# Kernel tuning notes

Hardware: AMD Instinct MI355X
Metric: run time of the kernel (lower is better)

Reference implementation:

```python
import jax, jax.numpy as jnp
import numpy as np

T_SCALE = 160
NUM_SAMPLE = 32
FEAT_DIM = 2048
HIDDEN = 512
N_CLASS = 20
BATCH = 8


def build_sample_mask(tscale=T_SCALE, ns=NUM_SAMPLE):
    # Vectorized version of _get_interp1d_mask (prop_boundary_ratio=0, num_sample_perbin=1).
    # Returns mask of shape [tscale, ns, start, end] (already transposed as in the torch code).
    s = np.arange(tscale)[:, None, None]           # start
    e = np.arange(tscale)[None, :, None]           # end
    k = np.arange(ns)[None, None, :]
    pos = s + (e - s) * k / (ns - 1.0)             # [T, T, ns] sample positions
    Sg, Eg, Kg = np.broadcast_arrays(s, e, k)
    posf = pos.ravel(); Sf = Sg.ravel(); Ef = Eg.ravel(); Kf = Kg.ravel()
    valid = Ef >= Sf
    frac, dn = np.modf(posf)
    dn = dn.astype(np.int64)
    up = np.ceil(posf).astype(np.int64)
    mask = np.zeros((tscale, ns, tscale, tscale), dtype=np.float32)
    m1 = valid & (dn >= 0) & (dn <= tscale - 1)
    np.add.at(mask, (dn[m1], Kf[m1], Sf[m1], Ef[m1]), (1.0 - frac[m1]).astype(np.float32))
    m2 = valid & (up >= 0) & (up <= tscale - 1)
    np.add.at(mask, (up[m2], Kf[m2], Sf[m2], Ef[m2]), frac[m2].astype(np.float32))
    return jnp.asarray(mask)


def conv1d(x, w, padding):
    # x: [B, Cin, T], w: [Cout, Cin, K]
    return jax.lax.conv_general_dilated(
        x, w, window_strides=(1,), padding=[(padding, padding)],
        dimension_numbers=("NCH", "OIH", "NCH"))


def setup_inputs() -> dict:
    key = jax.random.key(0)
    ks = jax.random.split(key, 6)
    x = jax.random.normal(ks[0], (BATCH, T_SCALE, FEAT_DIM), dtype=jnp.float32)
    w1 = jax.random.normal(ks[1], (HIDDEN, FEAT_DIM, 3), dtype=jnp.float32) * 0.02
    b1 = jnp.zeros((HIDDEN,), dtype=jnp.float32)
    wc = jax.random.normal(ks[2], (N_CLASS, HIDDEN, 1), dtype=jnp.float32) * 0.05
    wa = jax.random.normal(ks[3], (1, HIDDEN, 3), dtype=jnp.float32) * 0.05
    ba = jnp.zeros((1,), dtype=jnp.float32)
    sample_mask = build_sample_mask()  # [T, ns, T, T]
    return {"x": x, "sample_mask": sample_mask, "w1": w1, "b1": b1,
            "wc": wc, "wa": wa, "ba": ba}


def reference(x, sample_mask, w1, b1, wc, wa, ba):
    ns = NUM_SAMPLE
    q = ns // 4  # 8
    xp = jnp.transpose(x, (0, 2, 1))                   # [B, F, T]
    feat = jax.nn.relu(conv1d(xp, w1, 1) + b1[None, :, None])   # [B, H, T] (dropout = eval/identity)
    y_class = conv1d(feat, wc, 0)                      # [B, C, T]
    y_atn = conv1d(feat, wa, 1) + ba[None, :, None]    # [B, 1, T]
    # boundary matching: matmul against sparse interpolation mask
    out = jnp.einsum("bct,tkij->bckij", y_class, sample_mask)   # [B, C, ns, T, T]
    out_start = out[:, :, :q].mean(axis=2)
    out_mid = out[:, :, q:ns - q].mean(axis=2)
    out_end = out[:, :, ns - q:].mean(axis=2)
    bmn_class = jnp.concatenate((out_start, out_mid, out_end), axis=1)  # [B, 3C, T, T]
    sig = jax.nn.sigmoid(y_atn)
    x_fg = (sig * feat).sum(-1, keepdims=True) / (sig.sum(-1, keepdims=True) + 1e-8)  # [B, H, 1]
    y_fg = jnp.einsum("oh,bht->bot", wc[:, :, 0], x_fg)  # conv_class 1x1, no bias
    return (y_class, y_fg, bmn_class)
```

## Files before the change

kernel.cpp:

```cpp
#include <hip/hip_runtime.h>
#include <math.h>

#define TS 160
#define FEATD 2048
#define HID 512
#define NC 20
#define NB 8
#define KZ 8

typedef __attribute__((ext_vector_type(8))) short bfrag;
typedef __attribute__((ext_vector_type(4))) float f32x4;

static __device__ __forceinline__ unsigned short f2bf(float f) {
  unsigned int u = __float_as_uint(f);
  unsigned int r = (u + 0x7FFFu + ((u >> 16) & 1u)) >> 16;
  return (unsigned short)r;
}
static __device__ __forceinline__ float bf2f(unsigned short s) {
  return __uint_as_float(((unsigned int)s) << 16);
}

static __device__ __forceinline__ void gload16(const void* g, void* l) {
  __builtin_amdgcn_global_load_lds((const __attribute__((address_space(1))) void*)g,
                                   (__attribute__((address_space(3))) void*)l, 16, 0, 0);
}

__global__ __launch_bounds__(256) void k_prep(const float* __restrict__ x,
                                              const float* __restrict__ w1,
                                              const float* __restrict__ ba,
                                              unsigned short* __restrict__ xb,
                                              unsigned short* __restrict__ wb,
                                              unsigned short* __restrict__ WT,
                                              float* __restrict__ y_atn) {
  __shared__ float Ls[FEATD * 3];
  const int tid = threadIdx.x;
  const int bx = blockIdx.x;
  if (bx < 1296) {
    const int idx = bx * 256 + tid;
    const int c = (idx & 255) * 8;
    const int row = idx >> 8;
    const int b = row / 162, pr = row - b * 162;
    unsigned short* o = xb + (size_t)row * FEATD + c;
    if (pr == 0 || pr == 161) {
      *(uint4*)o = make_uint4(0u, 0u, 0u, 0u);
    } else {
      const float* src = x + ((size_t)(b * TS + pr - 1)) * FEATD + c;
      float4 v0 = *(const float4*)src;
      float4 v1 = *(const float4*)(src + 4);
      unsigned short r[8] = {f2bf(v0.x), f2bf(v0.y), f2bf(v0.z), f2bf(v0.w),
                             f2bf(v1.x), f2bf(v1.y), f2bf(v1.z), f2bf(v1.w)};
      *(uint4*)o = *(const uint4*)r;
    }
  } else if (bx < 1808) {
    const int h = bx - 1296;
    const float4* src = (const float4*)(w1 + (size_t)h * (FEATD * 3));
    for (int e = tid; e < FEATD * 3 / 4; e += 256) ((float4*)Ls)[e] = src[e];
    __syncthreads();
    for (int oc = tid; oc < 768; oc += 256) {
      const int tap = oc >> 8;
      const int f0 = (oc & 255) * 8;
      unsigned short r[8];
      #pragma unroll
      for (int i = 0; i < 8; ++i) r[i] = f2bf(Ls[(f0 + i) * 3 + tap]);
      *(uint4*)&wb[((size_t)tap * HID + h) * FEATD + f0] = *(const uint4*)r;
    }
  } else if (bx < 2408) {
    const int idx = (bx - 1808) * 256 + tid;
    const int tau = idx % 160;
    const int dd = (idx / 160) % 320;
    const int g = idx / (160 * 320);
    float w = 0.f;
    if (dd >= 160) {
      const int d = dd - 160;
      const int k0 = (g == 0) ? 0 : (g == 1 ? 8 : 24);
      const int k1 = (g == 0) ? 8 : (g == 1 ? 24 : 32);
      for (int k = k0; k < k1; ++k) {
        float p = (float)(d * k) / 31.0f;
        float a = fabsf(p - (float)tau);
        w += fmaxf(0.f, 1.f - a);
      }
      w *= (g == 1) ? 0.0625f : 0.125f;
    }
    WT[idx] = f2bf(w);
  } else {
    const int idx = (bx - 2408) * 256 + tid;
    if (idx < NB * TS) y_atn[idx] = ba[0];
  }
}

__global__ __launch_bounds__(256, 1) void k_conv_mfma(const unsigned short* __restrict__ xb,
                                                      const unsigned short* __restrict__ wb,
                                                      unsigned short* __restrict__ part) {
  const int bb = blockIdx.x;
  const int hq = blockIdx.y;
  const int kz = blockIdx.z;
  const int tid = threadIdx.x;
  const int wid = tid >> 6, lane = tid & 63;

  __shared__ unsigned short Alds[2][12288];
  __shared__ unsigned short Blds[2][24576];

  const unsigned short* xbb = xb + (size_t)bb * 162 * FEATD;

  f32x4 acc[5][4] = {};
  const int wr = wid >> 1, wc = wid & 1;

  auto STAGE = [&](int half, int s) {
    const int f0 = kz * 256 + s * 64;
    #pragma unroll
    for (int is = 0; is < 6; ++is) {
      const int ci = is * 256 + wid * 64 + lane;
      int row = ci >> 3;
      if (row > 161) row = 161;
      const int c = ci & 7;
      gload16(xbb + (size_t)row * FEATD + f0 + ((c ^ (row & 7)) << 3),
              (char*)Alds[half] + (size_t)(is * 256 + wid * 64) * 16);
    }
    #pragma unroll
    for (int is = 0; is < 12; ++is) {
      const int ci = is * 256 + wid * 64 + lane;
      const int tap = ci >> 10, rr = (ci >> 3) & 127, c = ci & 7;
      gload16(wb + ((size_t)(tap * HID + hq * 128 + rr)) * FEATD + f0 + ((c ^ (rr & 7)) << 3),
              (char*)Blds[half] + (size_t)(is * 256 + wid * 64) * 16);
    }
  };

  STAGE(0, 0);
  __syncthreads();

  int cur = 0;
  for (int s = 0; s < 4; ++s) {
    if (s < 3) STAGE(cur ^ 1, s + 1);
    #pragma unroll
    for (int tap = 0; tap < 3; ++tap) {
      #pragma unroll
      for (int kk = 0; kk < 2; ++kk) {
        const int cc = kk * 4 + (lane >> 4);
        bfrag bfr[4];
        #pragma unroll
        for (int nf = 0; nf < 4; ++nf) {
          const int hh = wc * 64 + nf * 16 + (lane & 15);
          bfr[nf] = *(const bfrag*)((char*)Blds[cur] + (size_t)(((tap * 128 + hh) * 8) + (cc ^ (hh & 7))) * 16);
        }
        #pragma unroll
        for (int mi = 0; mi < 5; ++mi) {
          const int rr = wr * 80 + mi * 16 + (lane & 15) + tap;
          bfrag af = *(const bfrag*)((char*)Alds[cur] + (size_t)((rr * 8) + (cc ^ (rr & 7))) * 16);
          #pragma unroll
          for (int nf = 0; nf < 4; ++nf)
            acc[mi][nf] = __builtin_amdgcn_mfma_f32_16x16x32_bf16(af, bfr[nf], acc[mi][nf], 0, 0, 0);
        }
      }
    }
    __syncthreads();
    cur ^= 1;
  }

  unsigned short* pout = part + (size_t)kz * (NB * TS) * HID;
  #pragma unroll
  for (int mi = 0; mi < 5; ++mi) {
    const int r0 = bb * TS + wr * 80 + mi * 16 + (lane >> 4) * 4;
    #pragma unroll
    for (int nf = 0; nf < 4; ++nf) {
      const int c0 = hq * 128 + wc * 64 + nf * 16 + (lane & 15);
      #pragma unroll
      for (int i = 0; i < 4; ++i)
        pout[(size_t)(r0 + i) * HID + c0] = f2bf(acc[mi][nf][i]);
    }
  }
}

__global__ __launch_bounds__(256) void k_feat_head(const unsigned short* __restrict__ part,
                                                   const float* __restrict__ b1,
                                                   const float* __restrict__ wc,
                                                   const float* __restrict__ wa,
                                                   float* __restrict__ feat,
                                                   float* __restrict__ y_class,
                                                   float* __restrict__ y_atn) {
  const int r0 = blockIdx.x * 4;
  const int tid = threadIdx.x;
  const int wv = tid >> 6, lane = tid & 63;
  __shared__ float fr[4][HID];
  __shared__ float sred[4][4][3];
  const int h0 = tid * 2;
  const float bb0 = b1[h0], bb1 = b1[h0 + 1];
  const float wa0 = wa[h0 * 3 + 0], wa1 = wa[h0 * 3 + 1], wa2 = wa[h0 * 3 + 2];
  const float wa3 = wa[h0 * 3 + 3], wa4 = wa[h0 * 3 + 4], wa5 = wa[h0 * 3 + 5];

  #pragma unroll
  for (int r = 0; r < 4; ++r) {
    const int bt = r0 + r;
    float a0 = bb0, a1 = bb1;
    #pragma unroll
    for (int kz = 0; kz < KZ; ++kz) {
      unsigned int v = *(const unsigned int*)&part[(size_t)kz * (NB * TS * HID) + (size_t)bt * HID + h0];
      a0 += bf2f((unsigned short)(v & 0xffff));
      a1 += bf2f((unsigned short)(v >> 16));
    }
    a0 = fmaxf(a0, 0.f);
    a1 = fmaxf(a1, 0.f);
    float2 fo; fo.x = a0; fo.y = a1;
    *(float2*)&feat[(size_t)bt * HID + h0] = fo;
    fr[r][h0] = a0; fr[r][h0 + 1] = a1;
    float s0 = a0 * wa0 + a1 * wa3;
    float s1 = a0 * wa1 + a1 * wa4;
    float s2 = a0 * wa2 + a1 * wa5;
    #pragma unroll
    for (int off = 32; off; off >>= 1) {
      s0 += __shfl_xor(s0, off);
      s1 += __shfl_xor(s1, off);
      s2 += __shfl_xor(s2, off);
    }
    if (lane == 0) { sred[r][wv][0] = s0; sred[r][wv][1] = s1; sred[r][wv][2] = s2; }
  }
  __syncthreads();

  #pragma unroll
  for (int r = 0; r < 4; ++r) {
    const int bt = r0 + r;
    const int b = bt / TS, t = bt - b * TS;
    for (int c = wv; c < NC; c += 4) {
      float p = 0.f;
      #pragma unroll
      for (int i2 = 0; i2 < 8; ++i2) p += fr[r][lane + 64 * i2] * wc[c * HID + lane + 64 * i2];
      #pragma unroll
      for (int off = 32; off; off >>= 1) p += __shfl_xor(p, off);
      if (lane == 0) y_class[((size_t)b * NC + c) * TS + t] = p;
    }
  }
  if (tid < 4) {
    const int bt = r0 + tid;
    const int t = bt % TS;
    float S0 = sred[tid][0][0] + sred[tid][1][0] + sred[tid][2][0] + sred[tid][3][0];
    float S1 = sred[tid][0][1] + sred[tid][1][1] + sred[tid][2][1] + sred[tid][3][1];
    float S2 = sred[tid][0][2] + sred[tid][1][2] + sred[tid][2][2] + sred[tid][3][2];
    atomicAdd(&y_atn[bt], S1);
    if (t < TS - 1) atomicAdd(&y_atn[bt + 1], S0);
    if (t > 0)      atomicAdd(&y_atn[bt - 1], S2);
  }
}

__global__ __launch_bounds__(256) void k_tail(const float* __restrict__ y_class,
                                              const unsigned short* __restrict__ WT,
                                              const float* __restrict__ feat,
                                              const float* __restrict__ y_atn,
                                              const float* __restrict__ wc,
                                              float* __restrict__ y_fg,
                                              float* __restrict__ bmn) {
  __shared__ char Tlds[64000 + 65536];
  const int tid = threadIdx.x;

  if (blockIdx.y == 3) {
    if (blockIdx.x >= NB) return;
    const int b = blockIdx.x;
    float* sig = (float*)Tlds;
    float* red = sig + TS;
    float* xfg = red + 8;
    float s = 0.f;
    if (tid < TS) { s = 1.f / (1.f + expf(-y_atn[b * TS + tid])); sig[tid] = s; }
    float r = s;
    #pragma unroll
    for (int off = 32; off; off >>= 1) r += __shfl_xor(r, off);
    if ((tid & 63) == 0) red[tid >> 6] = r;
    __syncthreads();
    const float inv = 1.f / (red[0] + red[1] + red[2] + red[3] + 1e-8f);
    for (int h = tid; h < HID; h += 256) {
      float a = 0.f;
      for (int t = 0; t < TS; ++t) a += sig[t] * feat[((size_t)b * TS + t) * HID + h];
      xfg[h] = a * inv;
    }
    __syncthreads();
    const int wv = tid >> 6, lane = tid & 63;
    for (int c = wv; c < NC; c += 4) {
      float p = 0.f;
      #pragma unroll
      for (int i2 = 0; i2 < 8; ++i2) {
        int h = lane + 64 * i2;
        p += wc[c * HID + h] * xfg[h];
      }
      #pragma unroll
      for (int off = 32; off; off >>= 1) p += __shfl_xor(p, off);
      if (lane == 0) y_fg[b * NC + c] = p;
    }
    return;
  }

  char* Alds = Tlds;
  char* Wlds = Tlds + 64000;
  const int i = blockIdx.x;
  const int g = blockIdx.y;
  const int wid = tid >> 6, lane = tid & 63;

  const char* wtb = (const char*)WT + (size_t)g * 102400 + (size_t)(160 - i) * 320;
  #pragma unroll
  for (int it = 0; it < 16; ++it) {
    const int idx = it * 256 + tid;
    int row = idx / 25, c = idx - row * 25;
    if (row > 159) row = 159;
    if (c > 19) c = 0;
    gload16(wtb + (size_t)row * 320 + c * 16, Wlds + (size_t)idx * 16);
  }
  for (int e = 0; e < 13; ++e) {
    const int ci = e * 256 + tid;
    if (ci < 3200) {
      const int row = ci / 20, c = ci - row * 20;
      const int tb = i + c * 8;
      const float* yr = y_class + (size_t)row * TS;
      unsigned short r8[8];
      #pragma unroll
      for (int k = 0; k < 8; ++k) {
        const int t = tb + k;
        r8[k] = (t < TS) ? f2bf(yr[t]) : (unsigned short)0;
      }
      *(uint4*)(Alds + (size_t)row * 400 + c * 16) = *(const uint4*)r8;
    }
  }
  __syncthreads();

  const int wr = wid >> 1, wcq = wid & 1;
  f32x4 acc[5][5] = {};

  #pragma unroll
  for (int ks = 0; ks < 5; ++ks) {
    const int cc = ks * 4 + (lane >> 4);
    bfrag bfr[5];
    #pragma unroll
    for (int nf = 0; nf < 5; ++nf) {
      const int j = wcq * 80 + nf * 16 + (lane & 15);
      bfr[nf] = *(const bfrag*)(Wlds + (size_t)j * 400 + cc * 16);
    }
    #pragma unroll
    for (int mf = 0; mf < 5; ++mf) {
      const int r = wr * 80 + mf * 16 + (lane & 15);
      bfrag af = *(const bfrag*)(Alds + (size_t)r * 400 + cc * 16);
      #pragma unroll
      for (int nf = 0; nf < 5; ++nf)
        acc[mf][nf] = __builtin_amdgcn_mfma_f32_16x16x32_bf16(af, bfr[nf], acc[mf][nf], 0, 0, 0);
    }
  }

  #pragma unroll
  for (int mf = 0; mf < 5; ++mf) {
    const int r0 = wr * 80 + mf * 16 + (lane >> 4) * 4;
    #pragma unroll
    for (int reg = 0; reg < 4; ++reg) {
      const int r = r0 + reg;
      const int b = r / 20, c = r - b * 20;
      float* base = bmn + (((size_t)(b * 60 + g * 20 + c) * TS) + i) * TS;
      #pragma unroll
      for (int nf = 0; nf < 5; ++nf) {
        const int j = wcq * 80 + nf * 16 + (lane & 15);
        base[j] = acc[mf][nf][reg];
      }
    }
  }
}

extern "C" void kernel_launch(void* const* d_in, const int* in_sizes, int n_in,
                              void* d_out, int out_size, void* d_ws, size_t ws_size,
                              hipStream_t stream) {
  const float* x  = (const float*)d_in[0];
  const float* w1 = (const float*)d_in[2];
  const float* b1 = (const float*)d_in[3];
  const float* wc = (const float*)d_in[4];
  const float* wa = (const float*)d_in[5];
  const float* ba = (const float*)d_in[6];

  float* out     = (float*)d_out;
  float* y_class = out;
  float* y_fg    = out + NB * NC * TS;
  float* bmn     = out + NB * NC * TS + NB * NC;

  unsigned short* part = (unsigned short*)d_ws;
  float* feat  = (float*)((char*)d_ws + (size_t)KZ * NB * TS * HID * 2);
  float* y_atn = feat + NB * TS * HID;
  unsigned short* xb = (unsigned short*)(y_atn + 2048);
  unsigned short* wb = xb + (size_t)NB * 162 * FEATD;
  unsigned short* WT = wb + (size_t)3 * HID * FEATD;

  k_prep<<<2413, 256, 0, stream>>>(x, w1, ba, xb, wb, WT, y_atn);
  k_conv_mfma<<<dim3(8, 4, KZ), 256, 0, stream>>>(xb, wb, part);
  k_feat_head<<<NB * TS / 4, 256, 0, stream>>>(part, b1, wc, wa, feat, y_class, y_atn);
  k_tail<<<dim3(160, 4), 256, 0, stream>>>(y_class, WT, feat, y_atn, wc, y_fg, bmn);
}
```

Baseline: 78.72 us.

## Split conv K further, drop double buffering, read tail weights from global

The conv kernel doubles its split-K factor, so each block covers 128 features in two single-buffered stages instead of four double-buffered ones. That cuts LDS enough to allow two blocks per CU under the new launch bounds; the two halo rows are now loaded with plain loads. The tail kernel stops staging the interpolation weight matrix in LDS and reads B fragments straight from global memory (through cache), halving LDS so two blocks can fit. The aim is more blocks and more occupancy, at the cost of losing load/compute overlap, writing twice as many partial sums for the feature reduction, and uncoalesced global fragment reads in the tail.

After: 69.90 us (median of 2 runs). 1.13x faster.

```diff
diff --git a/kernel.cpp b/kernel.cpp
--- a/kernel.cpp
+++ b/kernel.cpp
@@ -6,7 +6,7 @@
 #define HID 512
 #define NC 20
 #define NB 8
-#define KZ 8
+#define KZ 16
 
 typedef __attribute__((ext_vector_type(8))) short bfrag;
 typedef __attribute__((ext_vector_type(4))) float f32x4;
@@ -88,7 +88,7 @@
   }
 }
 
-__global__ __launch_bounds__(256, 1) void k_conv_mfma(const unsigned short* __restrict__ xb,
+__global__ __launch_bounds__(256, 2) void k_conv_mfma(const unsigned short* __restrict__ xb,
                                                       const unsigned short* __restrict__ wb,
                                                       unsigned short* __restrict__ part) {
   const int bb = blockIdx.x;
@@ -97,40 +97,37 @@
   const int tid = threadIdx.x;
   const int wid = tid >> 6, lane = tid & 63;
 
-  __shared__ unsigned short Alds[2][12288];
-  __shared__ unsigned short Blds[2][24576];
+  __shared__ unsigned short Alds[162 * 64];
+  __shared__ unsigned short Blds[3 * 128 * 64];
 
   const unsigned short* xbb = xb + (size_t)bb * 162 * FEATD;
 
   f32x4 acc[5][4] = {};
   const int wr = wid >> 1, wc = wid & 1;
 
-  auto STAGE = [&](int half, int s) {
-    const int f0 = kz * 256 + s * 64;
-    #pragma unroll
-    for (int is = 0; is < 6; ++is) {
+  for (int s = 0; s < 2; ++s) {
+    const int f0 = kz * 128 + s * 64;
+    #pragma unroll
+    for (int is = 0; is < 5; ++is) {
       const int ci = is * 256 + wid * 64 + lane;
-      int row = ci >> 3;
-      if (row > 161) row = 161;
-      const int c = ci & 7;
+      const int row = ci >> 3, c = ci & 7;
       gload16(xbb + (size_t)row * FEATD + f0 + ((c ^ (row & 7)) << 3),
-              (char*)Alds[half] + (size_t)(is * 256 + wid * 64) * 16);
+              (char*)Alds + (size_t)(is * 256 + wid * 64) * 16);
     }
     #pragma unroll
     for (int is = 0; is < 12; ++is) {
       const int ci = is * 256 + wid * 64 + lane;
       const int tap = ci >> 10, rr = (ci >> 3) & 127, c = ci & 7;
       gload16(wb + ((size_t)(tap * HID + hq * 128 + rr)) * FEATD + f0 + ((c ^ (rr & 7)) << 3),
-              (char*)Blds[half] + (size_t)(is * 256 + wid * 64) * 16);
-    }
-  };
-
-  STAGE(0, 0);
-  __syncthreads();
-
-  int cur = 0;
-  for (int s = 0; s < 4; ++s) {
-    if (s < 3) STAGE(cur ^ 1, s + 1);
+              (char*)Blds + (size_t)(is * 256 + wid * 64) * 16);
+    }
+    if (tid < 16) {
+      const int row = 160 + (tid >> 3), c = tid & 7;
+      uint4 v = *(const uint4*)(xbb + (size_t)row * FEATD + f0 + ((c ^ (row & 7)) << 3));
+      *(uint4*)((char*)Alds + row * 128 + c * 16) = v;
+    }
+    __syncthreads();
+
     #pragma unroll
     for (int tap = 0; tap < 3; ++tap) {
       #pragma unroll
@@ -140,12 +137,12 @@
         #pragma unroll
         for (int nf = 0; nf < 4; ++nf) {
           const int hh = wc * 64 + nf * 16 + (lane & 15);
-          bfr[nf] = *(const bfrag*)((char*)Blds[cur] + (size_t)(((tap * 128 + hh) * 8) + (cc ^ (hh & 7))) * 16);
+          bfr[nf] = *(const bfrag*)((char*)Blds + (size_t)(((tap * 128 + hh) * 8) + (cc ^ (hh & 7))) * 16);
         }
         #pragma unroll
         for (int mi = 0; mi < 5; ++mi) {
           const int rr = wr * 80 + mi * 16 + (lane & 15) + tap;
-          bfrag af = *(const bfrag*)((char*)Alds[cur] + (size_t)((rr * 8) + (cc ^ (rr & 7))) * 16);
+          bfrag af = *(const bfrag*)((char*)Alds + (size_t)((rr * 8) + (cc ^ (rr & 7))) * 16);
           #pragma unroll
           for (int nf = 0; nf < 4; ++nf)
             acc[mi][nf] = __builtin_amdgcn_mfma_f32_16x16x32_bf16(af, bfr[nf], acc[mi][nf], 0, 0, 0);
@@ -153,7 +150,6 @@
       }
     }
     __syncthreads();
-    cur ^= 1;
   }
 
   unsigned short* pout = part + (size_t)kz * (NB * TS) * HID;
@@ -240,20 +236,20 @@
   }
 }
 
-__global__ __launch_bounds__(256) void k_tail(const float* __restrict__ y_class,
-                                              const unsigned short* __restrict__ WT,
-                                              const float* __restrict__ feat,
-                                              const float* __restrict__ y_atn,
-                                              const float* __restrict__ wc,
-                                              float* __restrict__ y_fg,
-                                              float* __restrict__ bmn) {
-  __shared__ char Tlds[64000 + 65536];
+__global__ __launch_bounds__(256, 2) void k_tail(const float* __restrict__ y_class,
+                                                 const unsigned short* __restrict__ WT,
+                                                 const float* __restrict__ feat,
+                                                 const float* __restrict__ y_atn,
+                                                 const float* __restrict__ wc,
+                                                 float* __restrict__ y_fg,
+                                                 float* __restrict__ bmn) {
+  __shared__ char Alds[64000];
   const int tid = threadIdx.x;
 
   if (blockIdx.y == 3) {
     if (blockIdx.x >= NB) return;
     const int b = blockIdx.x;
-    float* sig = (float*)Tlds;
+    float* sig = (float*)Alds;
     float* red = sig + TS;
     float* xfg = red + 8;
     float s = 0.f;
@@ -285,21 +281,11 @@
     return;
   }
 
-  char* Alds = Tlds;
-  char* Wlds = Tlds + 64000;
   const int i = blockIdx.x;
   const int g = blockIdx.y;
   const int wid = tid >> 6, lane = tid & 63;
 
   const char* wtb = (const char*)WT + (size_t)g * 102400 + (size_t)(160 - i) * 320;
-  #pragma unroll
-  for (int it = 0; it < 16; ++it) {
-    const int idx = it * 256 + tid;
-    int row = idx / 25, c = idx - row * 25;
-    if (row > 159) row = 159;
-    if (c > 19) c = 0;
-    gload16(wtb + (size_t)row * 320 + c * 16, Wlds + (size_t)idx * 16);
-  }
   for (int e = 0; e < 13; ++e) {
     const int ci = e * 256 + tid;
     if (ci < 3200) {
@@ -327,7 +313,7 @@
     #pragma unroll
     for (int nf = 0; nf < 5; ++nf) {
       const int j = wcq * 80 + nf * 16 + (lane & 15);
-      bfr[nf] = *(const bfrag*)(Wlds + (size_t)j * 400 + cc * 16);
+      bfr[nf] = *(const bfrag*)(wtb + (size_t)j * 320 + cc * 16);
     }
     #pragma unroll
     for (int mf = 0; mf < 5; ++mf) {
```
